# Performance work log

Measured on AMD Instinct MI355X. Metric: run time of the kernel, lower is better.

## Reference

```python
import jax, jax.numpy as jnp
import numpy as np

B, C, H, W = 2, 512, 48, 48
HEADS = 8          # head_dim = C // HEADS = 64
GROUPS = 32        # min(32, ceil(512/4)) = 32
EPS = 1e-5


def setup_inputs() -> dict:
    key = jax.random.key(0)
    ks = jax.random.split(key, 5)
    return {
        "x": jax.random.normal(ks[0], (B, C, H, W), jnp.float32),
        "gn_w": jnp.ones((C,), jnp.float32),
        "gn_b": jnp.zeros((C,), jnp.float32),
        # 1x1 convs stored as [out, in] matrices
        "qkv_w": jax.random.normal(ks[1], (3 * C, C), jnp.float32) / np.float32(np.sqrt(C)),
        "qkv_b": jax.random.normal(ks[2], (3 * C,), jnp.float32) * 0.01,
        "proj_w": jax.random.normal(ks[3], (C, C), jnp.float32) / np.float32(np.sqrt(C)),
        "proj_b": jax.random.normal(ks[4], (C,), jnp.float32) * 0.01,
    }


def _group_norm(x, w, b):
    b_, c_, h_, w_ = x.shape
    xg = x.reshape(b_, GROUPS, c_ // GROUPS, h_, w_)
    mean = xg.mean(axis=(2, 3, 4), keepdims=True)
    var = xg.var(axis=(2, 3, 4), keepdims=True)  # biased, matches F.group_norm
    xn = ((xg - mean) * jax.lax.rsqrt(var + EPS)).reshape(b_, c_, h_, w_)
    return xn * w[None, :, None, None] + b[None, :, None, None]


def reference(x, gn_w, gn_b, qkv_w, qkv_b, proj_w, proj_b):
    bx, cx, hx, wx = x.shape
    d = cx // HEADS
    n = hx * wx
    xn = _group_norm(x, gn_w, gn_b)
    # qkv 1x1 conv -> [B, 3C, H, W]
    y = jnp.einsum('oc,bchw->bohw', qkv_w, xn) + qkv_b[None, :, None, None]
    # torch: y.reshape(B*heads, d, 3, N).unbind(2)  (channel layout: head, chan, qkv)
    qkv = y.reshape(bx * HEADS, d, 3, n)
    q, k, v = qkv[:, :, 0, :], qkv[:, :, 1, :], qkv[:, :, 2, :]
    scale = np.float32(1.0 / np.sqrt(d))
    # AttentionOp: fp32 QK^T + softmax over keys (axis=2)
    w_attn = jax.nn.softmax(jnp.einsum('ncq,nck->nqk', q, k * scale), axis=2)
    a = jnp.einsum('nqk,nck->ncq', w_attn, v).reshape(bx, cx, hx, wx)
    out = jnp.einsum('oc,bchw->bohw', proj_w, a) + proj_b[None, :, None, None]
    return out + x
```

## Files before the change

### kernel.cpp

```cpp
#include <hip/hip_runtime.h>

typedef __bf16 bf16;
typedef __bf16 bf16x8 __attribute__((ext_vector_type(8)));
typedef __bf16 bf16x4 __attribute__((ext_vector_type(4)));
typedef float f32x4 __attribute__((ext_vector_type(4)));

#define B_ 2
#define C_ 512
#define HW_ 2304
#define GROUPS_ 32
#define CPG_ 16
#define EPS_ 1e-5f
#define THR_ 8.0f
#define LOG2E_ 1.44269504f
#define EXP2(x) __builtin_amdgcn_exp2f(x)

__device__ __forceinline__ void gload_lds16(const bf16* g, bf16* l) {
  __builtin_amdgcn_global_load_lds((const __attribute__((address_space(1))) void*)g,
                                   (__attribute__((address_space(3))) void*)l, 16, 0, 0);
}

__global__ __launch_bounds__(256) void gn_stats_part_k(const float* __restrict__ x,
                                                       float* __restrict__ ps,
                                                       float* __restrict__ pss) {
  int blk = blockIdx.x;
  int bg = blk >> 3, seg = blk & 7;
  const int n4 = CPG_ * HW_ / 4 / 8;
  const float4* p = (const float4*)(x + (long)bg * CPG_ * HW_) + (long)seg * n4;
  float s = 0.f, ss = 0.f;
  for (int i = threadIdx.x; i < n4; i += 256) {
    float4 v = p[i];
    s += v.x + v.y + v.z + v.w;
    ss += v.x * v.x + v.y * v.y + v.z * v.z + v.w * v.w;
  }
#pragma unroll
  for (int d = 1; d < 64; d <<= 1) { s += __shfl_xor(s, d); ss += __shfl_xor(ss, d); }
  __shared__ float rs[4], rss[4];
  int wave = threadIdx.x >> 6, lane = threadIdx.x & 63;
  if (lane == 0) { rs[wave] = s; rss[wave] = ss; }
  __syncthreads();
  if (threadIdx.x == 0) {
    ps[blk] = rs[0] + rs[1] + rs[2] + rs[3];
    pss[blk] = rss[0] + rss[1] + rss[2] + rss[3];
  }
}

__global__ __launch_bounds__(256) void gn_apply_k(const float* __restrict__ x,
                                                  const float* __restrict__ gw,
                                                  const float* __restrict__ gb,
                                                  const float* __restrict__ ps,
                                                  const float* __restrict__ pss,
                                                  bf16* __restrict__ xnT) {
  int n0 = blockIdx.x * 64, c0 = blockIdx.y * 32, b = blockIdx.z;
  int nn = n0 + (threadIdx.x & 63);
  int cb = c0 + ((threadIdx.x >> 6) << 3);
  int gi = b * GROUPS_ + (cb >> 4);
  float s = 0.f, ss = 0.f;
#pragma unroll
  for (int k = 0; k < 8; ++k) { s += ps[gi * 8 + k]; ss += pss[gi * 8 + k]; }
  const float invN = 1.0f / (float)(CPG_ * HW_);
  float mu = s * invN;
  float var = ss * invN - mu * mu;
  float rstd = rsqrtf(var + EPS_);
  bf16x8 o;
#pragma unroll
  for (int j = 0; j < 8; ++j) {
    int c = cb + j;
    float sc = rstd * gw[c];
    float sh = gb[c] - mu * sc;
    float v = x[((long)b * C_ + c) * HW_ + nn];
    o[j] = (bf16)(v * sc + sh);
  }
  *(bf16x8*)&xnT[((long)b * HW_ + nn) * C_ + cb] = o;
}

__global__ __launch_bounds__(256) void prep_w_k(const float* __restrict__ qkv_w,
                                                const float* __restrict__ qkv_b,
                                                const float* __restrict__ proj_w,
                                                bf16* __restrict__ wqk,
                                                bf16* __restrict__ wv,
                                                bf16* __restrict__ wp,
                                                float* __restrict__ bqk,
                                                float* __restrict__ bv) {
  int idx = blockIdx.x * 256 + threadIdx.x;
  int r = idx >> 9, c = idx & 511;
  {
    int src = (r < 512) ? 3 * r : 3 * (r - 512) + 1;
    float sc = (r < 512) ? 0.125f * LOG2E_ : 1.0f;
    wqk[idx] = (bf16)(qkv_w[(long)src * 512 + c] * sc);
  }
  if (r < 512) {
    wv[idx] = (bf16)(qkv_w[(long)(3 * r + 2) * 512 + c]);
    wp[idx] = (bf16)(proj_w[idx]);
  }
  if (idx < 1024) {
    int src = (idx < 512) ? 3 * idx : 3 * (idx - 512) + 1;
    float sc = (idx < 512) ? 0.125f * LOG2E_ : 1.0f;
    bqk[idx] = qkv_b[src] * sc;
  }
  if (idx < 512) bv[idx] = qkv_b[3 * idx + 2];
}

template <int BIAS_MODE, bool RESID, typename OUT_T>
__global__ __launch_bounds__(256) void gemm_k(const bf16* __restrict__ A,
                                              const bf16* __restrict__ BT,
                                              const float* __restrict__ bias,
                                              const float* __restrict__ resid,
                                              OUT_T* __restrict__ Cc,
                                              int M, int N, int K,
                                              long sA, long sBT, long sC) {
  int b = blockIdx.z;
  A += sA * b;
  BT += sBT * b;
  Cc += sC * b;
  const float* R = RESID ? (resid + sC * b) : nullptr;
  int m0 = blockIdx.y * 64, n0 = blockIdx.x * 64;
  int tid = threadIdx.x, lane = tid & 63, wave = tid >> 6;
  int wm = (wave >> 1) << 5, wn = (wave & 1) << 5;
  int fr = lane & 15, kg = (lane >> 4) << 3;
  __shared__ __align__(16) bf16 As[2][64 * 32];
  __shared__ __align__(16) bf16 Bs[2][64 * 32];
  int sr = tid >> 2, sc = (tid & 3) << 3;
  const bf16* gA = A + (long)(m0 + sr) * K + sc;
  const bf16* gB = BT + (long)(n0 + sr) * K + sc;
  f32x4 acc[2][2] = {};
  const int NSTEP = K >> 5;
  gload_lds16(gA, &As[0][tid * 8]);
  gload_lds16(gB, &Bs[0][tid * 8]);
  __syncthreads();
  for (int t = 0; t < NSTEP; ++t) {
    int cur = t & 1;
    if (t + 1 < NSTEP) {
      int k0 = (t + 1) << 5;
      gload_lds16(gA + k0, &As[cur ^ 1][tid * 8]);
      gload_lds16(gB + k0, &Bs[cur ^ 1][tid * 8]);
    }
    bf16x8 a0 = *(bf16x8*)&As[cur][(wm + fr) * 32 + kg];
    bf16x8 a1 = *(bf16x8*)&As[cur][(wm + 16 + fr) * 32 + kg];
    bf16x8 b0 = *(bf16x8*)&Bs[cur][(wn + fr) * 32 + kg];
    bf16x8 b1 = *(bf16x8*)&Bs[cur][(wn + 16 + fr) * 32 + kg];
    acc[0][0] = __builtin_amdgcn_mfma_f32_16x16x32_bf16(a0, b0, acc[0][0], 0, 0, 0);
    acc[0][1] = __builtin_amdgcn_mfma_f32_16x16x32_bf16(a0, b1, acc[0][1], 0, 0, 0);
    acc[1][0] = __builtin_amdgcn_mfma_f32_16x16x32_bf16(a1, b0, acc[1][0], 0, 0, 0);
    acc[1][1] = __builtin_amdgcn_mfma_f32_16x16x32_bf16(a1, b1, acc[1][1], 0, 0, 0);
    __syncthreads();
  }
  int rbase = (lane >> 4) << 2;
#pragma unroll
  for (int mi = 0; mi < 2; ++mi)
#pragma unroll
    for (int nj = 0; nj < 2; ++nj)
#pragma unroll
      for (int reg = 0; reg < 4; ++reg) {
        int row = m0 + wm + (mi << 4) + rbase + reg;
        int col = n0 + wn + (nj << 4) + fr;
        float v = acc[mi][nj][reg];
        if (BIAS_MODE == 1) v += bias[row];
        if (BIAS_MODE == 2) v += bias[col];
        if (RESID) v += R[(long)row * N + col];
        Cc[(long)row * N + col] = (OUT_T)v;
      }
}

__global__ __launch_bounds__(512) void attn_k(const bf16* __restrict__ yT,
                                              const bf16* __restrict__ V,
                                              bf16* __restrict__ Op,
                                              float* __restrict__ Mp,
                                              float* __restrict__ Lp) {
  const int n = HW_;
  int bh = blockIdx.y, b = bh >> 3, h = bh & 7;
  int split = blockIdx.z;
  int q0 = blockIdx.x * 128;
  int kbeg = split * (n / 2);
  const int NT = (n / 2) / 64;
  int tid = threadIdx.x, lane = tid & 63, wave = tid >> 6;
  int fr = lane & 15, g = lane >> 4, kg = g << 3;
  const bf16* yTb = yT + (long)b * n * 1024;
  const bf16* Vb = V + ((long)b * C_ + h * 64) * n;
  const bf16* Kb = yTb + 512 + h * 64;

  int qrow = q0 + (wave << 4) + fr;
  const bf16* qp = yTb + (long)qrow * 1024 + h * 64;
  bf16x8 qf0 = *(const bf16x8*)(qp + kg);
  bf16x8 qf1 = *(const bf16x8*)(qp + 32 + kg);

  __shared__ __align__(16) bf16 Kt[2][64][64];
  __shared__ __align__(16) bf16 Vt[2][64][64];

  int o0 = ((g + fr) & 7) << 3;
  int o1 = ((4 + g + fr) & 7) << 3;

  float m_run = -1e30f, l_run = 0.f;
  f32x4 oacc[4] = {};

  int r0 = tid >> 3;
  int ck = tid & 7;
  int c0e = ck << 3;
  int pk = ((ck + r0) & 7) << 3;
  int vs = (c0e & 32) | ((c0e & 8) << 1) | ((c0e & 16) >> 2);
  int cv = vs >> 3, sub = vs & 7;
  int pv0 = (((cv + r0) & 7) << 3) + sub;
  int pv1 = (((cv + 1 + r0) & 7) << 3) + sub;

  const bf16* kptr = Kb + (long)(kbeg + r0) * 1024 + c0e;
  const bf16* vptr = Vb + (long)r0 * n + kbeg + c0e;
  uint4 rk = *(const uint4*)kptr;
  uint4 rv = *(const uint4*)vptr;
  *(uint4*)&Kt[0][r0][pk] = rk;
  *(uint2*)&Vt[0][r0][pv0] = make_uint2(rv.x, rv.y);
  *(uint2*)&Vt[0][r0][pv1] = make_uint2(rv.z, rv.w);
  kptr += 64 * 1024;
  vptr += 64;
  rk = *(const uint4*)kptr;
  rv = *(const uint4*)vptr;
  __syncthreads();

  for (int t = 0; t < NT; ++t) {
    int cur = t & 1;
    f32x4 s[4] = {};
#pragma unroll
    for (int nj = 0; nj < 4; ++nj) {
      bf16x8 kf0 = *(bf16x8*)&Kt[cur][(nj << 4) + fr][o0];
      bf16x8 kf1 = *(bf16x8*)&Kt[cur][(nj << 4) + fr][o1];
      s[nj] = __builtin_amdgcn_mfma_f32_16x16x32_bf16(kf0, qf0, s[nj], 0, 0, 0);
      s[nj] = __builtin_amdgcn_mfma_f32_16x16x32_bf16(kf1, qf1, s[nj], 0, 0, 0);
    }
    if (t + 1 < NT) {
      int nb = cur ^ 1;
      *(uint4*)&Kt[nb][r0][pk] = rk;
      *(uint2*)&Vt[nb][r0][pv0] = make_uint2(rv.x, rv.y);
      *(uint2*)&Vt[nb][r0][pv1] = make_uint2(rv.z, rv.w);
      if (t + 2 < NT) {
        kptr += 64 * 1024;
        vptr += 64;
        rk = *(const uint4*)kptr;
        rv = *(const uint4*)vptr;
      }
    }
    float pm = fmaxf(fmaxf(s[0][0], s[0][1]), fmaxf(s[0][2], s[0][3]));
#pragma unroll
    for (int nj = 1; nj < 4; ++nj)
      pm = fmaxf(pm, fmaxf(fmaxf(s[nj][0], s[nj][1]), fmaxf(s[nj][2], s[nj][3])));
    pm = fmaxf(pm, __shfl_xor(pm, 16));
    pm = fmaxf(pm, __shfl_xor(pm, 32));
    if (__any(pm > m_run + THR_)) {
      float mn = fmaxf(m_run, pm);
      float corr = EXP2(m_run - mn);
      m_run = mn;
      l_run *= corr;
#pragma unroll
      for (int dj = 0; dj < 4; ++dj)
#pragma unroll
        for (int r = 0; r < 4; ++r) oacc[dj][r] *= corr;
    }
    float ls = 0.f;
    bf16x8 pa0, pa1;
#pragma unroll
    for (int r = 0; r < 4; ++r) {
      float p0 = EXP2(s[0][r] - m_run);
      float p1 = EXP2(s[1][r] - m_run);
      float p2 = EXP2(s[2][r] - m_run);
      float p3 = EXP2(s[3][r] - m_run);
      ls += (p0 + p1) + (p2 + p3);
      pa0[r] = (bf16)p0;
      pa0[4 + r] = (bf16)p1;
      pa1[r] = (bf16)p2;
      pa1[4 + r] = (bf16)p3;
    }
    ls += __shfl_xor(ls, 16);
    ls += __shfl_xor(ls, 32);
    l_run += ls;
#pragma unroll
    for (int dj = 0; dj < 4; ++dj) {
      bf16x8 vf0 = *(bf16x8*)&Vt[cur][(dj << 4) + fr][o0];
      bf16x8 vf1 = *(bf16x8*)&Vt[cur][(dj << 4) + fr][o1];
      oacc[dj] = __builtin_amdgcn_mfma_f32_16x16x32_bf16(vf0, pa0, oacc[dj], 0, 0, 0);
      oacc[dj] = __builtin_amdgcn_mfma_f32_16x16x32_bf16(vf1, pa1, oacc[dj], 0, 0, 0);
    }
    __syncthreads();
  }
  long orow = (long)(split * 16 + bh) * n + q0 + (wave << 4) + fr;
#pragma unroll
  for (int dj = 0; dj < 4; ++dj) {
    bf16x4 ov = {(bf16)oacc[dj][0], (bf16)oacc[dj][1], (bf16)oacc[dj][2], (bf16)oacc[dj][3]};
    *(bf16x4*)&Op[orow * 64 + (dj << 4) + (g << 2)] = ov;
  }
  if (g == 0) {
    Mp[orow] = m_run;
    Lp[orow] = l_run;
  }
}

__global__ __launch_bounds__(256) void attn_merge_k(const bf16* __restrict__ Op,
                                                    const float* __restrict__ Mp,
                                                    const float* __restrict__ Lp,
                                                    bf16* __restrict__ aT) {
  int bh = blockIdx.y, b = bh >> 3, h = bh & 7;
  int gi = blockIdx.x * 256 + threadIdx.x;
  int nrow = gi >> 3, dd8 = (gi & 7) << 3;
  long i0 = (long)bh * HW_ + nrow;
  long i1 = (long)(16 + bh) * HW_ + nrow;
  float m0 = Mp[i0], m1 = Mp[i1];
  float m = fmaxf(m0, m1);
  float e0 = EXP2(m0 - m), e1 = EXP2(m1 - m);
  float l = Lp[i0] * e0 + Lp[i1] * e1;
  float w0 = e0 / l, w1 = e1 / l;
  bf16x8 o0 = *(const bf16x8*)&Op[i0 * 64 + dd8];
  bf16x8 o1 = *(const bf16x8*)&Op[i1 * 64 + dd8];
  bf16x8 o;
#pragma unroll
  for (int j = 0; j < 8; ++j) o[j] = (bf16)((float)o0[j] * w0 + (float)o1[j] * w1);
  *(bf16x8*)&aT[((long)b * HW_ + nrow) * C_ + h * 64 + dd8] = o;
}

extern "C" void kernel_launch(void* const* d_in, const int* in_sizes, int n_in,
                              void* d_out, int out_size, void* d_ws, size_t ws_size,
                              hipStream_t stream) {
  const float* x = (const float*)d_in[0];
  const float* gn_w = (const float*)d_in[1];
  const float* gn_b = (const float*)d_in[2];
  const float* qkv_w = (const float*)d_in[3];
  const float* qkv_b = (const float*)d_in[4];
  const float* proj_w = (const float*)d_in[5];
  const float* proj_b = (const float*)d_in[6];
  float* out = (float*)d_out;

  char* ws = (char*)d_ws;
  float* ps = (float*)ws;   ws += 2048;
  float* pss = (float*)ws;  ws += 2048;
  float* bqk = (float*)ws;  ws += 4096;
  float* bv = (float*)ws;   ws += 2048;
  bf16* wqk = (bf16*)ws;    ws += 1024l * 512 * 2;
  bf16* wv = (bf16*)ws;     ws += 512l * 512 * 2;
  bf16* wp = (bf16*)ws;     ws += 512l * 512 * 2;
  bf16* xnT = (bf16*)ws;    ws += 2l * HW_ * 512 * 2;
  bf16* yT = (bf16*)ws;     ws += 2l * HW_ * 1024 * 2;
  bf16* v = (bf16*)ws;      ws += 2l * 512 * HW_ * 2;
  bf16* aT = (bf16*)ws;     ws += 2l * HW_ * 512 * 2;
  bf16* Op = (bf16*)ws;     ws += 2l * 16 * HW_ * 64 * 2;
  float* Mp = (float*)ws;   ws += 2l * 16 * HW_ * 4;
  float* Lp = (float*)ws;   ws += 2l * 16 * HW_ * 4;

  gn_stats_part_k<<<512, 256, 0, stream>>>(x, ps, pss);
  prep_w_k<<<2048, 256, 0, stream>>>(qkv_w, qkv_b, proj_w, wqk, wv, wp, bqk, bv);
  gn_apply_k<<<dim3(36, 16, 2), 256, 0, stream>>>(x, gn_w, gn_b, ps, pss, xnT);
  gemm_k<2, false, bf16><<<dim3(16, 36, 2), 256, 0, stream>>>(
      xnT, wqk, bqk, nullptr, yT, 2304, 1024, 512, (long)HW_ * 512, 0, (long)HW_ * 1024);
  gemm_k<1, false, bf16><<<dim3(36, 8, 2), 256, 0, stream>>>(
      wv, xnT, bv, nullptr, v, 512, 2304, 512, 0, (long)HW_ * 512, 512l * HW_);
  attn_k<<<dim3(18, 16, 2), 512, 0, stream>>>(yT, v, Op, Mp, Lp);
  attn_merge_k<<<dim3(72, 16), 256, 0, stream>>>(Op, Mp, Lp, aT);
  gemm_k<1, true, float><<<dim3(36, 8, 2), 256, 0, stream>>>(
      wp, aT, proj_b, x, out, 512, 2304, 512, 0, (long)HW_ * 512, 512l * HW_);
}
```

Before: 95.67 us.

## Split attention keys four ways, triple-buffer GEMM loads, raise MFMA wave priority

The attention kernel gets a template split count and switches to four key splits when the workspace is large enough. This doubles the grid from 576 to 1152 blocks, which should fill the GPU better, and the merge kernel now combines NS partial results. The GEMM hard-codes K=512, fully unrolls its loop, and moves to a three-stage LDS pipeline using explicit vmcnt waits and raw barriers, which cuts per-step synchronisation stalls. The attention MFMA sections are also wrapped in s_setprio. The trade-off is twice the partial-output traffic, more merge work, and GEMM code that only works for K=512.

New measurement: 93.93 us. No clear change (-1.8%).

```diff
diff --git a/kernel.cpp b/kernel.cpp
--- a/kernel.cpp
+++ b/kernel.cpp
@@ -107,8 +107,10 @@
                                               const float* __restrict__ bias,
                                               const float* __restrict__ resid,
                                               OUT_T* __restrict__ Cc,
-                                              int M, int N, int K,
+                                              int M, int N,
                                               long sA, long sBT, long sC) {
+  constexpr int KK = 512;
+  constexpr int NSTEP = KK >> 5;
   int b = blockIdx.z;
   A += sA * b;
   BT += sBT * b;
@@ -118,22 +120,26 @@
   int tid = threadIdx.x, lane = tid & 63, wave = tid >> 6;
   int wm = (wave >> 1) << 5, wn = (wave & 1) << 5;
   int fr = lane & 15, kg = (lane >> 4) << 3;
-  __shared__ __align__(16) bf16 As[2][64 * 32];
-  __shared__ __align__(16) bf16 Bs[2][64 * 32];
+  __shared__ __align__(16) bf16 As[3][64 * 32];
+  __shared__ __align__(16) bf16 Bs[3][64 * 32];
   int sr = tid >> 2, sc = (tid & 3) << 3;
-  const bf16* gA = A + (long)(m0 + sr) * K + sc;
-  const bf16* gB = BT + (long)(n0 + sr) * K + sc;
+  const bf16* gA = A + (long)(m0 + sr) * KK + sc;
+  const bf16* gB = BT + (long)(n0 + sr) * KK + sc;
   f32x4 acc[2][2] = {};
-  const int NSTEP = K >> 5;
   gload_lds16(gA, &As[0][tid * 8]);
   gload_lds16(gB, &Bs[0][tid * 8]);
-  __syncthreads();
+  gload_lds16(gA + 32, &As[1][tid * 8]);
+  gload_lds16(gB + 32, &Bs[1][tid * 8]);
+  asm volatile("s_waitcnt vmcnt(2)" ::: "memory");
+  __builtin_amdgcn_s_barrier();
+#pragma unroll
   for (int t = 0; t < NSTEP; ++t) {
-    int cur = t & 1;
-    if (t + 1 < NSTEP) {
-      int k0 = (t + 1) << 5;
-      gload_lds16(gA + k0, &As[cur ^ 1][tid * 8]);
-      gload_lds16(gB + k0, &Bs[cur ^ 1][tid * 8]);
+    const int cur = t % 3;
+    if (t + 2 < NSTEP) {
+      const int nb = (t + 2) % 3;
+      int k0 = (t + 2) << 5;
+      gload_lds16(gA + k0, &As[nb][tid * 8]);
+      gload_lds16(gB + k0, &Bs[nb][tid * 8]);
     }
     bf16x8 a0 = *(bf16x8*)&As[cur][(wm + fr) * 32 + kg];
     bf16x8 a1 = *(bf16x8*)&As[cur][(wm + 16 + fr) * 32 + kg];
@@ -143,7 +149,12 @@
     acc[0][1] = __builtin_amdgcn_mfma_f32_16x16x32_bf16(a0, b1, acc[0][1], 0, 0, 0);
     acc[1][0] = __builtin_amdgcn_mfma_f32_16x16x32_bf16(a1, b0, acc[1][0], 0, 0, 0);
     acc[1][1] = __builtin_amdgcn_mfma_f32_16x16x32_bf16(a1, b1, acc[1][1], 0, 0, 0);
-    __syncthreads();
+    if (t + 2 < NSTEP) {
+      asm volatile("s_waitcnt vmcnt(2) lgkmcnt(0)" ::: "memory");
+    } else if (t + 1 < NSTEP) {
+      asm volatile("s_waitcnt vmcnt(0) lgkmcnt(0)" ::: "memory");
+    }
+    if (t + 1 < NSTEP) __builtin_amdgcn_s_barrier();
   }
   int rbase = (lane >> 4) << 2;
 #pragma unroll
@@ -162,17 +173,18 @@
       }
 }
 
+template <int NS>
 __global__ __launch_bounds__(512) void attn_k(const bf16* __restrict__ yT,
                                               const bf16* __restrict__ V,
                                               bf16* __restrict__ Op,
                                               float* __restrict__ Mp,
                                               float* __restrict__ Lp) {
   const int n = HW_;
+  constexpr int NT = (HW_ / NS) / 64;
   int bh = blockIdx.y, b = bh >> 3, h = bh & 7;
   int split = blockIdx.z;
   int q0 = blockIdx.x * 128;
-  int kbeg = split * (n / 2);
-  const int NT = (n / 2) / 64;
+  int kbeg = split * (n / NS);
   int tid = threadIdx.x, lane = tid & 63, wave = tid >> 6;
   int fr = lane & 15, g = lane >> 4, kg = g << 3;
   const bf16* yTb = yT + (long)b * n * 1024;
@@ -218,6 +230,7 @@
   for (int t = 0; t < NT; ++t) {
     int cur = t & 1;
     f32x4 s[4] = {};
+    __builtin_amdgcn_s_setprio(1);
 #pragma unroll
     for (int nj = 0; nj < 4; ++nj) {
       bf16x8 kf0 = *(bf16x8*)&Kt[cur][(nj << 4) + fr][o0];
@@ -225,6 +238,7 @@
       s[nj] = __builtin_amdgcn_mfma_f32_16x16x32_bf16(kf0, qf0, s[nj], 0, 0, 0);
       s[nj] = __builtin_amdgcn_mfma_f32_16x16x32_bf16(kf1, qf1, s[nj], 0, 0, 0);
     }
+    __builtin_amdgcn_s_setprio(0);
     if (t + 1 < NT) {
       int nb = cur ^ 1;
       *(uint4*)&Kt[nb][r0][pk] = rk;
@@ -270,6 +284,7 @@
     ls += __shfl_xor(ls, 16);
     ls += __shfl_xor(ls, 32);
     l_run += ls;
+    __builtin_amdgcn_s_setprio(1);
 #pragma unroll
     for (int dj = 0; dj < 4; ++dj) {
       bf16x8 vf0 = *(bf16x8*)&Vt[cur][(dj << 4) + fr][o0];
@@ -277,6 +292,7 @@
       oacc[dj] = __builtin_amdgcn_mfma_f32_16x16x32_bf16(vf0, pa0, oacc[dj], 0, 0, 0);
       oacc[dj] = __builtin_amdgcn_mfma_f32_16x16x32_bf16(vf1, pa1, oacc[dj], 0, 0, 0);
     }
+    __builtin_amdgcn_s_setprio(0);
     __syncthreads();
   }
   long orow = (long)(split * 16 + bh) * n + q0 + (wave << 4) + fr;
@@ -291,6 +307,7 @@
   }
 }
 
+template <int NS>
 __global__ __launch_bounds__(256) void attn_merge_k(const bf16* __restrict__ Op,
                                                     const float* __restrict__ Mp,
                                                     const float* __restrict__ Lp,
@@ -298,18 +315,31 @@
   int bh = blockIdx.y, b = bh >> 3, h = bh & 7;
   int gi = blockIdx.x * 256 + threadIdx.x;
   int nrow = gi >> 3, dd8 = (gi & 7) << 3;
-  long i0 = (long)bh * HW_ + nrow;
-  long i1 = (long)(16 + bh) * HW_ + nrow;
-  float m0 = Mp[i0], m1 = Mp[i1];
-  float m = fmaxf(m0, m1);
-  float e0 = EXP2(m0 - m), e1 = EXP2(m1 - m);
-  float l = Lp[i0] * e0 + Lp[i1] * e1;
-  float w0 = e0 / l, w1 = e1 / l;
-  bf16x8 o0 = *(const bf16x8*)&Op[i0 * 64 + dd8];
-  bf16x8 o1 = *(const bf16x8*)&Op[i1 * 64 + dd8];
+  long idx[NS];
+  float mm = -1e30f;
+#pragma unroll
+  for (int s = 0; s < NS; ++s) {
+    idx[s] = (long)(s * 16 + bh) * HW_ + nrow;
+    mm = fmaxf(mm, Mp[idx[s]]);
+  }
+  float l = 0.f, w[NS];
+#pragma unroll
+  for (int s = 0; s < NS; ++s) {
+    w[s] = EXP2(Mp[idx[s]] - mm);
+    l += Lp[idx[s]] * w[s];
+  }
+  float invl = 1.f / l;
+  float oaccf[8] = {};
+#pragma unroll
+  for (int s = 0; s < NS; ++s) {
+    bf16x8 o = *(const bf16x8*)&Op[idx[s] * 64 + dd8];
+    float ws = w[s] * invl;
+#pragma unroll
+    for (int j = 0; j < 8; ++j) oaccf[j] += (float)o[j] * ws;
+  }
   bf16x8 o;
 #pragma unroll
-  for (int j = 0; j < 8; ++j) o[j] = (bf16)((float)o0[j] * w0 + (float)o1[j] * w1);
+  for (int j = 0; j < 8; ++j) o[j] = (bf16)oaccf[j];
   *(bf16x8*)&aT[((long)b * HW_ + nrow) * C_ + h * 64 + dd8] = o;
 }
 
@@ -337,19 +367,28 @@
   bf16* yT = (bf16*)ws;     ws += 2l * HW_ * 1024 * 2;
   bf16* v = (bf16*)ws;      ws += 2l * 512 * HW_ * 2;
   bf16* aT = (bf16*)ws;     ws += 2l * HW_ * 512 * 2;
-  bf16* Op = (bf16*)ws;     ws += 2l * 16 * HW_ * 64 * 2;
-  float* Mp = (float*)ws;   ws += 2l * 16 * HW_ * 4;
-  float* Lp = (float*)ws;   ws += 2l * 16 * HW_ * 4;
+  bf16* Op = (bf16*)ws;
+  size_t base_used = (size_t)(ws - (char*)d_ws);
+  size_t need4 = base_used + 4ull * 16 * HW_ * 64 * 2 + 2ull * 4 * 16 * HW_ * 4;
+  int NS = (ws_size >= need4) ? 4 : 2;
+  ws += (size_t)NS * 16 * HW_ * 64 * 2;
+  float* Mp = (float*)ws;   ws += (size_t)NS * 16 * HW_ * 4;
+  float* Lp = (float*)ws;   ws += (size_t)NS * 16 * HW_ * 4;
 
   gn_stats_part_k<<<512, 256, 0, stream>>>(x, ps, pss);
   prep_w_k<<<2048, 256, 0, stream>>>(qkv_w, qkv_b, proj_w, wqk, wv, wp, bqk, bv);
   gn_apply_k<<<dim3(36, 16, 2), 256, 0, stream>>>(x, gn_w, gn_b, ps, pss, xnT);
   gemm_k<2, false, bf16><<<dim3(16, 36, 2), 256, 0, stream>>>(
-      xnT, wqk, bqk, nullptr, yT, 2304, 1024, 512, (long)HW_ * 512, 0, (long)HW_ * 1024);
+      xnT, wqk, bqk, nullptr, yT, 2304, 1024, (long)HW_ * 512, 0, (long)HW_ * 1024);
   gemm_k<1, false, bf16><<<dim3(36, 8, 2), 256, 0, stream>>>(
-      wv, xnT, bv, nullptr, v, 512, 2304, 512, 0, (long)HW_ * 512, 512l * HW_);
-  attn_k<<<dim3(18, 16, 2), 512, 0, stream>>>(yT, v, Op, Mp, Lp);
-  attn_merge_k<<<dim3(72, 16), 256, 0, stream>>>(Op, Mp, Lp, aT);
+      wv, xnT, bv, nullptr, v, 512, 2304, 0, (long)HW_ * 512, 512l * HW_);
+  if (NS == 4) {
+    attn_k<4><<<dim3(18, 16, 4), 512, 0, stream>>>(yT, v, Op, Mp, Lp);
+    attn_merge_k<4><<<dim3(72, 16), 256, 0, stream>>>(Op, Mp, Lp, aT);
+  } else {
+    attn_k<2><<<dim3(18, 16, 2), 512, 0, stream>>>(yT, v, Op, Mp, Lp);
+    attn_merge_k<2><<<dim3(72, 16), 256, 0, stream>>>(Op, Mp, Lp, aT);
+  }
   gemm_k<1, true, float><<<dim3(36, 8, 2), 256, 0, stream>>>(
-      wp, aT, proj_b, x, out, 512, 2304, 512, 0, (long)HW_ * 512, 512l * HW_);
-}
+      wp, aT, proj_b, x, out, 512, 2304, 0, (long)HW_ * 512, 512l * HW_);
+}
```
